# Kernel optimization log

Hardware: AMD Instinct MI355X
Metric: run time of the kernel (lower is better)

The kernel has to match this reference:

```python
import jax, jax.numpy as jnp
import numpy as np

V = 49688; D = 128; Hd = 256; DM = 2 * Hd; FF = 4 * Hd; NH = 4
B = 256; O = 32; L = 32

def _ln(x, g, b, eps=1e-5):
    m = x.mean(-1, keepdims=True)
    v = x.var(-1, keepdims=True)
    return (x - m) / jnp.sqrt(v + eps) * g + b

def _mha(x, in_w, in_b, out_w, out_b, nh):
    Bx, S, E = x.shape
    hd = E // nh
    qkv = x @ in_w.T + in_b
    q, k, v = jnp.split(qkv, 3, axis=-1)
    sp = lambda t: t.reshape(Bx, S, nh, hd).transpose(0, 2, 1, 3)
    q, k, v = sp(q), sp(k), sp(v)
    s = jnp.einsum('bhqd,bhkd->bhqk', q, k) / jnp.sqrt(jnp.asarray(hd, x.dtype))
    o = jnp.einsum('bhqk,bhkd->bhqd', jax.nn.softmax(s, -1), v)
    o = o.transpose(0, 2, 1, 3).reshape(Bx, S, E)
    return o @ out_w.T + out_b

def _gru_dir(x, wih, whh, bih, bhh):
    Bx, T, _ = x.shape
    H = whh.shape[1]
    def step(h, xt):
        gi = xt @ wih.T + bih
        gh = h @ whh.T + bhh
        ir, iz, inn = jnp.split(gi, 3, -1)
        hr, hz, hn = jnp.split(gh, 3, -1)
        r = jax.nn.sigmoid(ir + hr)
        z = jax.nn.sigmoid(iz + hz)
        n = jnp.tanh(inn + r * hn)
        h = (1 - z) * n + z * h
        return h, h
    _, hs = jax.lax.scan(step, jnp.zeros((Bx, H), x.dtype), jnp.swapaxes(x, 0, 1))
    return jnp.swapaxes(hs, 0, 1)

def setup_inputs():
    key = jax.random.key(0)
    it = iter(jax.random.split(key, 48))
    def nrm(shape, s=0.05):
        return jax.random.normal(next(it), shape, jnp.float32) * s
    inp = {}
    inp['order_history'] = jax.random.randint(next(it), (B, O, L), 0, V + 1)
    inp['days_between'] = jax.random.uniform(next(it), (B, O - 1), jnp.float32) * 30.0
    inp['days_since_last'] = jax.random.uniform(next(it), (B,), jnp.float32) * 30.0
    inp['emb'] = nrm((V + 1, D), 1.0).at[0].set(0.0)  # padding_idx=0 -> zero row
    inp['a_in_w'] = nrm((3 * D, D)); inp['a_in_b'] = jnp.zeros((3 * D,))
    inp['a_out_w'] = nrm((D, D)); inp['a_out_b'] = jnp.zeros((D,))
    for d in ('f', 'b'):
        inp['g_wih_' + d] = nrm((3 * Hd, D)); inp['g_whh_' + d] = nrm((3 * Hd, Hd))
        inp['g_bih_' + d] = jnp.zeros((3 * Hd,)); inp['g_bhh_' + d] = jnp.zeros((3 * Hd,))
    inp['t_in_w'] = nrm((3 * DM, DM)); inp['t_in_b'] = jnp.zeros((3 * DM,))
    inp['t_out_w'] = nrm((DM, DM)); inp['t_out_b'] = jnp.zeros((DM,))
    inp['t_ln1_g'] = jnp.ones((DM,)); inp['t_ln1_b'] = jnp.zeros((DM,))
    inp['t_ff1_w'] = nrm((FF, DM)); inp['t_ff1_b'] = jnp.zeros((FF,))
    inp['t_ff2_w'] = nrm((DM, FF)); inp['t_ff2_b'] = jnp.zeros((DM,))
    inp['t_ln2_g'] = jnp.ones((DM,)); inp['t_ln2_b'] = jnp.zeros((DM,))
    inp['te1_w'] = nrm((Hd // 4, 2)); inp['te1_b'] = jnp.zeros((Hd // 4,))
    inp['te_ln1_g'] = jnp.ones((Hd // 4,)); inp['te_ln1_b'] = jnp.zeros((Hd // 4,))
    inp['te2_w'] = nrm((Hd // 2, Hd // 4)); inp['te2_b'] = jnp.zeros((Hd // 2,))
    inp['te_ln2_g'] = jnp.ones((Hd // 2,)); inp['te_ln2_b'] = jnp.zeros((Hd // 2,))
    inp['c_w'] = nrm((Hd, 2 * Hd + Hd // 2)); inp['c_b'] = jnp.zeros((Hd,))
    inp['c_ln_g'] = jnp.ones((Hd,)); inp['c_ln_b'] = jnp.zeros((Hd,))
    return inp

def reference(order_history, days_between, days_since_last, emb, a_in_w, a_in_b, a_out_w, a_out_b, g_wih_f, g_whh_f, g_bih_f, g_bhh_f, g_wih_b, g_whh_b, g_bih_b, g_bhh_b, t_in_w, t_in_b, t_out_w, t_out_b, t_ln1_g, t_ln1_b, t_ff1_w, t_ff1_b, t_ff2_w, t_ff2_b, t_ln2_g, t_ln2_b, te1_w, te1_b, te_ln1_g, te_ln1_b, te2_w, te2_b, te_ln2_g, te_ln2_b, c_w, c_b, c_ln_g, c_ln_b):
    Bx, Ox, Lx = order_history.shape
    # per-order item self-attention, batched over all (user, order) pairs
    x = emb[order_history].reshape(Bx * Ox, Lx, -1)                  # [B*O, L, D]
    x = _mha(x, a_in_w, a_in_b, a_out_w, a_out_b, NH)
    order_emb = x.mean(1).reshape(Bx, Ox, -1)                        # [B, O, D]
    # bidirectional GRU over the order sequence
    hf = _gru_dir(order_emb, g_wih_f, g_whh_f, g_bih_f, g_bhh_f)
    hb = _gru_dir(order_emb[:, ::-1], g_wih_b, g_whh_b, g_bih_b, g_bhh_b)[:, ::-1]
    g = jnp.concatenate([hf, hb], -1)                                # [B, O, 2H]
    # post-LN TransformerEncoderLayer (relu, dropout in eval mode)
    a = _mha(g, t_in_w, t_in_b, t_out_w, t_out_b, NH)
    g = _ln(g + a, t_ln1_g, t_ln1_b)
    f = jax.nn.relu(g @ t_ff1_w.T + t_ff1_b) @ t_ff2_w.T + t_ff2_b
    g = _ln(g + f, t_ln2_g, t_ln2_b)
    enc = g.mean(1)                                                  # [B, 2H]
    # temporal features: only days_mean and recency are used (std computed but unused in original)
    feats = jnp.stack([days_between.mean(1), days_since_last], 1)    # [B, 2]
    te = jax.nn.relu(_ln(feats @ te1_w.T + te1_b, te_ln1_g, te_ln1_b))
    te = jax.nn.relu(_ln(te @ te2_w.T + te2_b, te_ln2_g, te_ln2_b))  # [B, H/2]
    out = jax.nn.relu(_ln(jnp.concatenate([enc, te], 1) @ c_w.T + c_b, c_ln_g, c_ln_b))
    return out                                                       # [B, H]
```

## Files before the change

### kernel.cpp

```cpp
#include <hip/hip_runtime.h>
#include <hip/hip_bf16.h>
#include <math.h>

typedef __hip_bfloat16 bf16;
typedef __attribute__((ext_vector_type(8))) short short8v;
typedef __attribute__((ext_vector_type(4))) short short4v;
typedef __attribute__((ext_vector_type(4))) float float4v;
#define MFMA16 __builtin_amdgcn_mfma_f32_16x16x32_bf16

__device__ __forceinline__ float us2f(unsigned short u) {
  union { unsigned u; float f; } c; c.u = ((unsigned)u) << 16; return c.f;
}
__device__ __forceinline__ unsigned short f2us(float f) {
  return __bfloat16_as_ushort(__float2bfloat16(f));
}

__device__ __forceinline__ float dot_ff(const float* __restrict__ x,
                                        const float* __restrict__ w, int K) {
  const float4* xp = reinterpret_cast<const float4*>(x);
  const float4* wp = reinterpret_cast<const float4*>(w);
  float acc = 0.f;
  const int n = K >> 2;
  for (int i = 0; i < n; ++i) {
    float4 a = xp[i], b = wp[i];
    acc += a.x*b.x + a.y*b.y + a.z*b.z + a.w*b.w;
  }
  return acc;
}

__device__ __forceinline__ float sigm(float x) { return 1.f / (1.f + expf(-x)); }

__global__ void k_canary(float* __restrict__ out) {
  out[blockIdx.x * 256 + threadIdx.x] = 100.0f;
}

__global__ __launch_bounds__(256) void k_cvt(
    const float* __restrict__ a_in_w, const float* __restrict__ t_in_w,
    const float* __restrict__ t_out_w, const float* __restrict__ t_ff1w,
    const float* __restrict__ t_ff2w, const float* __restrict__ a_out_w,
    unsigned short* __restrict__ awb, unsigned short* __restrict__ twb,
    unsigned short* __restrict__ pwb, unsigned short* __restrict__ f1wb,
    unsigned short* __restrict__ f2wb, unsigned short* __restrict__ awb2)
{
  int i = blockIdx.x * 256 + threadIdx.x;
  if (i < 49152)  awb[i] = f2us(a_in_w[i]);
  if (i < 786432) twb[i] = f2us(t_in_w[i]);
  if (i < 262144) pwb[i] = f2us(t_out_w[i]);
  if (i < 524288) f1wb[i] = f2us(t_ff1w[i]);
  if (i < 524288) f2wb[i] = f2us(t_ff2w[i]);
  if (i < 16384)  awb2[i] = f2us(a_out_w[i]);
}

__global__ __launch_bounds__(256) void k_gru_wb(
    const float* __restrict__ wih_f, const float* __restrict__ whh_f,
    const float* __restrict__ wih_b, const float* __restrict__ whh_b,
    unsigned short* __restrict__ whhb, unsigned short* __restrict__ wihb)
{
  int i = blockIdx.x * 256 + threadIdx.x;
  if (i >= 393216) return;
  int dir = i / 196608, r = i % 196608;
  whhb[i] = f2us((dir ? whh_b : whh_f)[r]);
  if (r < 98304) wihb[dir * 98304 + r] = f2us((dir ? wih_b : wih_f)[r]);
}

__global__ __launch_bounds__(256, 4) void k_order_attn(
    const int* __restrict__ oh, const float* __restrict__ emb,
    const unsigned short* __restrict__ awb, const float* __restrict__ in_b,
    const unsigned short* __restrict__ awb2, const float* __restrict__ out_b,
    float* __restrict__ order_emb)
{
  const int bo = blockIdx.x;
  const int tid = threadIdx.x;
  __shared__ int ids[32];
  __shared__ alignas(16) unsigned short xs[32 * 136];
  __shared__ alignas(16) unsigned short qb[32 * 136];
  __shared__ alignas(16) unsigned short kb[32 * 136];
  __shared__ alignas(16) unsigned short vT[128 * 40];
  unsigned short* pb = xs;
  unsigned short* ob = qb;

  const int lane = tid & 63, wave = tid >> 6;
  const int l15 = lane & 15, quad = lane >> 4;

  if (tid < 32) ids[tid] = oh[bo * 32 + tid];
  __syncthreads();
  for (int i = tid; i < 1024; i += 256) {
    int t = i >> 5, d4 = (i & 31) << 2;
    float4 e4 = *reinterpret_cast<const float4*>(emb + (size_t)ids[t] * 128 + d4);
    short4v s; s[0] = f2us(e4.x); s[1] = f2us(e4.y); s[2] = f2us(e4.z); s[3] = f2us(e4.w);
    *reinterpret_cast<short4v*>(xs + t * 136 + d4) = s;
  }
  __syncthreads();
  {
    short8v af[2][4];
#pragma unroll
    for (int mt = 0; mt < 2; ++mt)
#pragma unroll
      for (int kc = 0; kc < 4; ++kc)
        af[mt][kc] = *reinterpret_cast<const short8v*>(
            xs + (mt * 16 + l15) * 136 + kc * 32 + quad * 8);
    for (int ni = 0; ni < 6; ++ni) {
      const int j = (wave + ni * 4) * 16 + l15;
      const unsigned short* wrow = awb + (size_t)j * 128;
      float4v acc0 = {0.f, 0.f, 0.f, 0.f}, acc1 = {0.f, 0.f, 0.f, 0.f};
#pragma unroll
      for (int kc = 0; kc < 4; ++kc) {
        short8v bfr = *reinterpret_cast<const short8v*>(wrow + kc * 32 + quad * 8);
        acc0 = MFMA16(af[0][kc], bfr, acc0, 0, 0, 0);
        acc1 = MFMA16(af[1][kc], bfr, acc1, 0, 0, 0);
      }
      const float bj = in_b[j];
      const int jj = j & 127;
      if (j < 256) {
        unsigned short* dst = (j < 128) ? qb : kb;
#pragma unroll
        for (int r = 0; r < 4; ++r) {
          int t0 = quad * 4 + r;
          dst[t0 * 136 + jj] = f2us(acc0[r] + bj);
          dst[(t0 + 16) * 136 + jj] = f2us(acc1[r] + bj);
        }
      } else {
        short4v s0, s1;
#pragma unroll
        for (int r = 0; r < 4; ++r) { s0[r] = f2us(acc0[r] + bj); s1[r] = f2us(acc1[r] + bj); }
        *reinterpret_cast<short4v*>(vT + jj * 40 + quad * 4) = s0;
        *reinterpret_cast<short4v*>(vT + jj * 40 + 16 + quad * 4) = s1;
      }
    }
  }
  __syncthreads();
  {
    const int h = wave;
    const float scale1 = 0.17677669529663687f;
    short8v qf[2], kf[2];
#pragma unroll
    for (int mt = 0; mt < 2; ++mt)
      qf[mt] = *reinterpret_cast<const short8v*>(qb + (mt * 16 + l15) * 136 + h * 32 + quad * 8);
#pragma unroll
    for (int nt = 0; nt < 2; ++nt)
      kf[nt] = *reinterpret_cast<const short8v*>(kb + (nt * 16 + l15) * 136 + h * 32 + quad * 8);
    float4v sacc[2][2];
#pragma unroll
    for (int mt = 0; mt < 2; ++mt)
#pragma unroll
      for (int nt = 0; nt < 2; ++nt) {
        sacc[mt][nt] = (float4v){0.f, 0.f, 0.f, 0.f};
        sacc[mt][nt] = MFMA16(qf[mt], kf[nt], sacc[mt][nt], 0, 0, 0);
      }
    float inv_reg[2][4];
#pragma unroll
    for (int mt = 0; mt < 2; ++mt)
#pragma unroll
      for (int r = 0; r < 4; ++r) {
        float s0 = sacc[mt][0][r] * scale1;
        float s1 = sacc[mt][1][r] * scale1;
        float mx = fmaxf(s0, s1);
        mx = fmaxf(mx, __shfl_xor(mx, 1));
        mx = fmaxf(mx, __shfl_xor(mx, 2));
        mx = fmaxf(mx, __shfl_xor(mx, 4));
        mx = fmaxf(mx, __shfl_xor(mx, 8));
        float e0 = expf(s0 - mx), e1 = expf(s1 - mx);
        float sm = e0 + e1;
        sm += __shfl_xor(sm, 1);
        sm += __shfl_xor(sm, 2);
        sm += __shfl_xor(sm, 4);
        sm += __shfl_xor(sm, 8);
        inv_reg[mt][r] = 1.f / sm;
        int row = h * 32 + mt * 16 + quad * 4 + r;
        pb[row * 32 + l15] = f2us(e0);
        pb[row * 32 + 16 + l15] = f2us(e1);
      }
    short8v pf[2], vf[2];
#pragma unroll
    for (int mt = 0; mt < 2; ++mt)
      pf[mt] = *reinterpret_cast<const short8v*>(pb + (h * 32 + mt * 16 + l15) * 32 + quad * 8);
#pragma unroll
    for (int nt = 0; nt < 2; ++nt)
      vf[nt] = *reinterpret_cast<const short8v*>(vT + (h * 32 + nt * 16 + l15) * 40 + quad * 8);
    float4v oacc[2][2];
#pragma unroll
    for (int mt = 0; mt < 2; ++mt)
#pragma unroll
      for (int nt = 0; nt < 2; ++nt) {
        oacc[mt][nt] = (float4v){0.f, 0.f, 0.f, 0.f};
        oacc[mt][nt] = MFMA16(pf[mt], vf[nt], oacc[mt][nt], 0, 0, 0);
      }
#pragma unroll
    for (int mt = 0; mt < 2; ++mt)
#pragma unroll
      for (int r = 0; r < 4; ++r) {
        int t = mt * 16 + quad * 4 + r;
        float inv = inv_reg[mt][r];
#pragma unroll
        for (int nt = 0; nt < 2; ++nt)
          ob[t * 136 + h * 32 + nt * 16 + l15] = f2us(oacc[mt][nt][r] * inv);
      }
  }
  __syncthreads();
  {
    float4v acc[2][2];
#pragma unroll
    for (int mt = 0; mt < 2; ++mt)
#pragma unroll
      for (int nt = 0; nt < 2; ++nt) acc[mt][nt] = (float4v){0.f, 0.f, 0.f, 0.f};
#pragma unroll
    for (int kc = 0; kc < 4; ++kc) {
      short8v af0 = *reinterpret_cast<const short8v*>(ob + l15 * 136 + kc * 32 + quad * 8);
      short8v af1 = *reinterpret_cast<const short8v*>(ob + (16 + l15) * 136 + kc * 32 + quad * 8);
#pragma unroll
      for (int nt = 0; nt < 2; ++nt) {
        int j = (wave * 2 + nt) * 16 + l15;
        short8v bfr = *reinterpret_cast<const short8v*>(awb2 + (size_t)j * 128 + kc * 32 + quad * 8);
        acc[0][nt] = MFMA16(af0, bfr, acc[0][nt], 0, 0, 0);
        acc[1][nt] = MFMA16(af1, bfr, acc[1][nt], 0, 0, 0);
      }
    }
#pragma unroll
    for (int nt = 0; nt < 2; ++nt) {
      float part = 0.f;
#pragma unroll
      for (int mt = 0; mt < 2; ++mt)
#pragma unroll
        for (int r = 0; r < 4; ++r) part += acc[mt][nt][r];
      part += __shfl_xor(part, 16);
      part += __shfl_xor(part, 32);
      if (quad == 0) {
        int j = (wave * 2 + nt) * 16 + l15;
        order_emb[(size_t)bo * 128 + j] = part * (1.f / 32.f) + out_b[j];
      }
    }
  }
}

__global__ __launch_bounds__(256, 2) void k_gru_gi(
    const float* __restrict__ oe, const unsigned short* __restrict__ wihb,
    unsigned short* __restrict__ gi)
{
  const int row0 = blockIdx.x * 32, tid = threadIdx.x;
  __shared__ alignas(16) unsigned short xs[32 * 136];
  for (int i = tid; i < 32 * 128; i += 256) {
    int t = i >> 7, d = i & 127;
    xs[t * 136 + d] = f2us(oe[(size_t)(row0 + t) * 128 + d]);
  }
  __syncthreads();
  const int lane = tid & 63, wave = tid >> 6;
  const int l15 = lane & 15, quad = lane >> 4;
  short8v af[2][4];
#pragma unroll
  for (int mt = 0; mt < 2; ++mt)
#pragma unroll
    for (int kc = 0; kc < 4; ++kc)
      af[mt][kc] = *reinterpret_cast<const short8v*>(
          xs + (mt * 16 + l15) * 136 + kc * 32 + quad * 8);
  for (int ni = 0; ni < 24; ++ni) {
    int col = (wave + ni * 4) * 16 + l15;
    const unsigned short* wrow = wihb + (size_t)col * 128;
    float4v a0 = {0.f,0.f,0.f,0.f}, a1 = {0.f,0.f,0.f,0.f};
#pragma unroll
    for (int kc = 0; kc < 4; ++kc) {
      short8v bfr = *reinterpret_cast<const short8v*>(wrow + kc * 32 + quad * 8);
      a0 = MFMA16(af[0][kc], bfr, a0, 0, 0, 0);
      a1 = MFMA16(af[1][kc], bfr, a1, 0, 0, 0);
    }
#pragma unroll
    for (int r = 0; r < 4; ++r) {
      gi[(size_t)(row0 + quad * 4 + r) * 1536 + col] = f2us(a0[r]);
      gi[(size_t)(row0 + quad * 4 + r + 16) * 1536 + col] = f2us(a1[r]);
    }
  }
}

__global__ __launch_bounds__(512, 2) void k_gru_rec(
    const unsigned short* __restrict__ gi, const unsigned short* __restrict__ whhb,
    const float* __restrict__ bih_f, const float* __restrict__ bhh_f,
    const float* __restrict__ bih_b, const float* __restrict__ bhh_b,
    float* __restrict__ g)
{
  const int b0 = blockIdx.x * 2, dir = blockIdx.y;
  const int tid = threadIdx.x;
  const unsigned short* wb = whhb + (size_t)dir * 196608;
  const float* bih = dir ? bih_b : bih_f;
  const float* bhh = dir ? bhh_b : bhh_f;
  __shared__ alignas(16) unsigned short hb[16 * 264];
  __shared__ float pg[2 * 772];
  const int lane = tid & 63, wave = tid >> 6;
  const int l15 = lane & 15, quad = lane >> 4;
  const int j = tid & 255, mb = tid >> 8;
  const float bir = bih[j], biz = bih[256 + j], bin_ = bih[512 + j];
  const float bhr = bhh[j], bhz = bhh[256 + j], bhn  = bhh[512 + j];
  short8v wf[6][8];
  int cols[6];
#pragma unroll
  for (int ni = 0; ni < 6; ++ni) {
    cols[ni] = (wave + ni * 8) * 16 + l15;
#pragma unroll
    for (int kc = 0; kc < 8; ++kc)
      wf[ni][kc] = *reinterpret_cast<const short8v*>(
          wb + (size_t)cols[ni] * 256 + kc * 32 + quad * 8);
  }
  for (int i = tid; i < 16 * 264; i += 512) hb[i] = 0;
  {
    int t0 = dir ? 31 : 0;
    size_t gb0 = ((size_t)(b0 + mb) * 32 + t0) * 1536 + dir * 768;
    (void)gb0;
  }
  int tcur = dir ? 31 : 0;
  size_t gbase = ((size_t)(b0 + mb) * 32 + tcur) * 1536 + dir * 768;
  float gr = us2f(gi[gbase + j]);
  float gz = us2f(gi[gbase + 256 + j]);
  float gn = us2f(gi[gbase + 512 + j]);
  __syncthreads();
  for (int s = 0; s < 32; ++s) {
    float4v acc[6];
#pragma unroll
    for (int ni = 0; ni < 6; ++ni) acc[ni] = (float4v){0.f, 0.f, 0.f, 0.f};
#pragma unroll
    for (int kc = 0; kc < 8; ++kc) {
      short8v af = *reinterpret_cast<const short8v*>(hb + l15 * 264 + kc * 32 + quad * 8);
#pragma unroll
      for (int ni = 0; ni < 6; ++ni)
        acc[ni] = MFMA16(af, wf[ni][kc], acc[ni], 0, 0, 0);
    }
    if (quad == 0) {
#pragma unroll
      for (int ni = 0; ni < 6; ++ni) {
        pg[cols[ni]] = acc[ni][0];
        pg[772 + cols[ni]] = acc[ni][1];
      }
    }
    float gr2 = 0.f, gz2 = 0.f, gn2 = 0.f;
    if (s < 31) {
      int t2 = dir ? (30 - s) : (s + 1);
      size_t gb2 = ((size_t)(b0 + mb) * 32 + t2) * 1536 + dir * 768;
      gr2 = us2f(gi[gb2 + j]);
      gz2 = us2f(gi[gb2 + 256 + j]);
      gn2 = us2f(gi[gb2 + 512 + j]);
    }
    __syncthreads();
    {
      const int tt = dir ? (31 - s) : s;
      float hprev = us2f(hb[mb * 264 + j]);
      float r = sigm(gr + bir + pg[mb * 772 + j] + bhr);
      float z = sigm(gz + biz + pg[mb * 772 + 256 + j] + bhz);
      float n = tanhf(gn + bin_ + r * (pg[mb * 772 + 512 + j] + bhn));
      float nh = (1.f - z) * n + z * hprev;
      hb[mb * 264 + j] = f2us(nh);
      g[((size_t)(b0 + mb) * 32 + tt) * 512 + dir * 256 + j] = nh;
    }
    gr = gr2; gz = gz2; gn = gn2;
    __syncthreads();
  }
}

#define XS2_STR 264

__global__ __launch_bounds__(256, 3) void k_mha2f(
    const float* __restrict__ g, const unsigned short* __restrict__ twb,
    const float* __restrict__ Bv, float* __restrict__ attn)
{
  const int b = blockIdx.x, h = blockIdx.y, tid = threadIdx.x;
  __shared__ alignas(16) unsigned short xs2[32 * XS2_STR];
  __shared__ alignas(16) unsigned short qk[2 * 32 * 136];
  __shared__ alignas(16) unsigned short vT[128 * 40];
  unsigned short* qs = qk;
  unsigned short* ks = qk + 32 * 136;
  float* sc = reinterpret_cast<float*>(xs2);
  unsigned short* pb = xs2 + 2112;
  const int lane = tid & 63, wave = tid >> 6;
  const int l15 = lane & 15, quad = lane >> 4;

  int wrowi[6];
#pragma unroll
  for (int ni = 0; ni < 6; ++ni) {
    int idx = (wave + ni * 4) * 16 + l15;
    int m = idx >> 7, dd = idx & 127;
    wrowi[ni] = m * 512 + h * 128 + dd;
  }
  float4v acc[6][2];
#pragma unroll
  for (int ni = 0; ni < 6; ++ni)
#pragma unroll
    for (int mt = 0; mt < 2; ++mt) acc[ni][mt] = (float4v){0.f, 0.f, 0.f, 0.f};

  for (int half = 0; half < 2; ++half) {
    __syncthreads();
    for (int i = tid; i < 2048; i += 256) {
      int t = i >> 6, c4 = (i & 63) << 2;
      float4 e4 = *reinterpret_cast<const float4*>(
          g + (size_t)b * 16384 + t * 512 + half * 256 + c4);
      short4v s; s[0] = f2us(e4.x); s[1] = f2us(e4.y); s[2] = f2us(e4.z); s[3] = f2us(e4.w);
      *reinterpret_cast<short4v*>(xs2 + t * XS2_STR + c4) = s;
    }
    __syncthreads();
    for (int kl = 0; kl < 2; ++kl) {
      const int kg = half * 2 + kl;
      short8v af[2][4];
#pragma unroll
      for (int mt = 0; mt < 2; ++mt)
#pragma unroll
        for (int u = 0; u < 4; ++u)
          af[mt][u] = *reinterpret_cast<const short8v*>(
              xs2 + (mt * 16 + l15) * XS2_STR + kl * 128 + u * 32 + quad * 8);
#pragma unroll
      for (int ni = 0; ni < 6; ++ni) {
        const unsigned short* wrow = twb + (size_t)wrowi[ni] * 512 + kg * 128;
#pragma unroll
        for (int u = 0; u < 4; ++u) {
          short8v bfr = *reinterpret_cast<const short8v*>(wrow + u * 32 + quad * 8);
          acc[ni][0] = MFMA16(af[0][u], bfr, acc[ni][0], 0, 0, 0);
          acc[ni][1] = MFMA16(af[1][u], bfr, acc[ni][1], 0, 0, 0);
        }
      }
    }
  }
#pragma unroll
  for (int ni = 0; ni < 6; ++ni) {
    int idx = (wave + ni * 4) * 16 + l15;
    int m = idx >> 7, dd = idx & 127;
    float bj = Bv[wrowi[ni]];
    if (m < 2) {
      unsigned short* dst = (m == 0) ? qs : ks;
#pragma unroll
      for (int r = 0; r < 4; ++r) {
        int t0 = quad * 4 + r;
        dst[t0 * 136 + dd] = f2us(acc[ni][0][r] + bj);
        dst[(t0 + 16) * 136 + dd] = f2us(acc[ni][1][r] + bj);
      }
    } else {
      short4v s0, s1;
#pragma unroll
      for (int r = 0; r < 4; ++r) { s0[r] = f2us(acc[ni][0][r] + bj); s1[r] = f2us(acc[ni][1][r] + bj); }
      *reinterpret_cast<short4v*>(vT + dd * 40 + quad * 4) = s0;
      *reinterpret_cast<short4v*>(vT + dd * 40 + 16 + quad * 4) = s1;
    }
  }
  __syncthreads();
  {
    const float scale2 = 0.08838834764831845f;
    const int mt = wave >> 1, nt = wave & 1;
    float4v a = {0.f, 0.f, 0.f, 0.f};
#pragma unroll
    for (int kc = 0; kc < 4; ++kc) {
      short8v qf = *reinterpret_cast<const short8v*>(qs + (mt * 16 + l15) * 136 + kc * 32 + quad * 8);
      short8v kf = *reinterpret_cast<const short8v*>(ks + (nt * 16 + l15) * 136 + kc * 32 + quad * 8);
      a = MFMA16(qf, kf, a, 0, 0, 0);
    }
#pragma unroll
    for (int r = 0; r < 4; ++r)
      sc[(mt * 16 + quad * 4 + r) * 33 + nt * 16 + l15] = a[r] * scale2;
  }
  __syncthreads();
  if (tid < 128) {
    int row = tid >> 2, seg = tid & 3;
    float* srow = sc + row * 33;
    float mx = srow[seg * 8];
#pragma unroll
    for (int c = 1; c < 8; ++c) mx = fmaxf(mx, srow[seg * 8 + c]);
    mx = fmaxf(mx, __shfl_xor(mx, 1));
    mx = fmaxf(mx, __shfl_xor(mx, 2));
    float s = 0.f;
    short8v pv;
#pragma unroll
    for (int c = 0; c < 8; ++c) {
      float e = expf(srow[seg * 8 + c] - mx);
      s += e; pv[c] = f2us(e);
    }
    *reinterpret_cast<short8v*>(pb + row * 32 + seg * 8) = pv;
    s += __shfl_xor(s, 1);
    s += __shfl_xor(s, 2);
    if (seg == 0) srow[32] = 1.f / s;
  }
  __syncthreads();
  {
    short8v pf[2], vf[2];
#pragma unroll
    for (int mt = 0; mt < 2; ++mt)
      pf[mt] = *reinterpret_cast<const short8v*>(pb + (mt * 16 + l15) * 32 + quad * 8);
#pragma unroll
    for (int ntl = 0; ntl < 2; ++ntl)
      vf[ntl] = *reinterpret_cast<const short8v*>(vT + ((2 * wave + ntl) * 16 + l15) * 40 + quad * 8);
    float4v oacc[2][2];
#pragma unroll
    for (int mt = 0; mt < 2; ++mt)
#pragma unroll
      for (int ntl = 0; ntl < 2; ++ntl) {
        oacc[mt][ntl] = (float4v){0.f, 0.f, 0.f, 0.f};
        oacc[mt][ntl] = MFMA16(pf[mt], vf[ntl], oacc[mt][ntl], 0, 0, 0);
      }
#pragma unroll
    for (int mt = 0; mt < 2; ++mt)
#pragma unroll
      for (int r = 0; r < 4; ++r) {
        int q = mt * 16 + quad * 4 + r;
        float inv = sc[q * 33 + 32];
#pragma unroll
        for (int ntl = 0; ntl < 2; ++ntl)
          attn[((size_t)b * 32 + q) * 512 + h * 128 + (2 * wave + ntl) * 16 + l15] =
              oacc[mt][ntl][r] * inv;
      }
  }
}

__global__ __launch_bounds__(256, 2) void k_projln_mfma(
    const float* __restrict__ X, const unsigned short* __restrict__ Wb,
    const float* __restrict__ bias, const float* __restrict__ res,
    const float* __restrict__ gam, const float* __restrict__ bet,
    float* __restrict__ Y)
{
  const int row0 = blockIdx.x * 16, tid = threadIdx.x;
  __shared__ alignas(16) unsigned short xs[16 * 520];
  __shared__ float ys[16 * 516];
  for (int i = tid; i < 16 * 512; i += 256) {
    int t = i >> 9, c = i & 511;
    xs[t * 520 + c] = f2us(X[(size_t)(row0 + t) * 512 + c]);
  }
  __syncthreads();
  {
    const int lane = tid & 63, wave = tid >> 6;
    const int l15 = lane & 15, quad = lane >> 4;
    short8v af[16];
#pragma unroll
    for (int kc = 0; kc < 16; ++kc)
      af[kc] = *reinterpret_cast<const short8v*>(xs + l15 * 520 + kc * 32 + quad * 8);
    for (int ni = 0; ni < 8; ++ni) {
      int col = (wave + ni * 4) * 16 + l15;
      const unsigned short* wrow = Wb + (size_t)col * 512;
      float4v acc = {0.f,0.f,0.f,0.f};
#pragma unroll
      for (int kc = 0; kc < 16; ++kc) {
        short8v bfr = *reinterpret_cast<const short8v*>(wrow + kc * 32 + quad * 8);
        acc = MFMA16(af[kc], bfr, acc, 0, 0, 0);
      }
      float bj = bias[col];
#pragma unroll
      for (int r = 0; r < 4; ++r)
        ys[(quad * 4 + r) * 516 + col] = acc[r] + bj;
    }
  }
  __syncthreads();
  for (int i = tid; i < 16 * 512; i += 256) {
    int t = i >> 9, c = i & 511;
    ys[t * 516 + c] += res[(size_t)(row0 + t) * 512 + c];
  }
  __syncthreads();
  {
    int row = tid >> 4, l16 = tid & 15;
    const float* yr = ys + row * 516;
    float part = 0.f;
#pragma unroll
    for (int k = 0; k < 32; ++k) part += yr[l16 + 16 * k];
#pragma unroll
    for (int off = 8; off; off >>= 1) part += __shfl_xor(part, off, 16);
    float mean = part * (1.f / 512.f);
    float var = 0.f;
#pragma unroll
    for (int k = 0; k < 32; ++k) { float d = yr[l16 + 16 * k] - mean; var += d * d; }
#pragma unroll
    for (int off = 8; off; off >>= 1) var += __shfl_xor(var, off, 16);
    float rs = rsqrtf(var * (1.f / 512.f) + 1e-5f);
    for (int k = 0; k < 32; ++k) {
      int c = l16 + 16 * k;
      Y[(size_t)(row0 + row) * 512 + c] = (yr[c] - mean) * rs * gam[c] + bet[c];
    }
  }
}

__global__ __launch_bounds__(256, 2) void k_ff1_mfma(
    const float* __restrict__ X, const unsigned short* __restrict__ Wb,
    const float* __restrict__ bias, unsigned short* __restrict__ Y)
{
  const int row0 = blockIdx.x * 16, tid = threadIdx.x;
  __shared__ alignas(16) unsigned short xs[16 * 520];
  for (int i = tid; i < 16 * 512; i += 256) {
    int t = i >> 9, c = i & 511;
    xs[t * 520 + c] = f2us(X[(size_t)(row0 + t) * 512 + c]);
  }
  __syncthreads();
  const int lane = tid & 63, wave = tid >> 6;
  const int l15 = lane & 15, quad = lane >> 4;
  short8v af[16];
#pragma unroll
  for (int kc = 0; kc < 16; ++kc)
    af[kc] = *reinterpret_cast<const short8v*>(xs + l15 * 520 + kc * 32 + quad * 8);
  for (int ni = 0; ni < 16; ++ni) {
    int col = (wave + ni * 4) * 16 + l15;
    const unsigned short* wrow = Wb + (size_t)col * 512;
    float4v acc = {0.f,0.f,0.f,0.f};
#pragma unroll
    for (int kc = 0; kc < 16; ++kc) {
      short8v bfr = *reinterpret_cast<const short8v*>(wrow + kc * 32 + quad * 8);
      acc = MFMA16(af[kc], bfr, acc, 0, 0, 0);
    }
    float bj = bias[col];
#pragma unroll
    for (int r = 0; r < 4; ++r)
      Y[(size_t)(row0 + quad * 4 + r) * 1024 + col] = f2us(fmaxf(acc[r] + bj, 0.f));
  }
}

__global__ __launch_bounds__(256, 2) void k_ff2ln_mfma(
    const unsigned short* __restrict__ X, const unsigned short* __restrict__ Wb,
    const float* __restrict__ bias, const float* __restrict__ res,
    const float* __restrict__ gam, const float* __restrict__ bet,
    float* __restrict__ Y)
{
  const int row0 = blockIdx.x * 16, tid = threadIdx.x;
  __shared__ alignas(16) unsigned short xs[16 * 520];
  __shared__ float ys[16 * 516];
  const int lane = tid & 63, wave = tid >> 6;
  const int l15 = lane & 15, quad = lane >> 4;
  float4v acc[8];
#pragma unroll
  for (int ni = 0; ni < 8; ++ni) acc[ni] = (float4v){0.f,0.f,0.f,0.f};
  for (int half = 0; half < 2; ++half) {
    __syncthreads();
    for (int i = tid; i < 16 * 512; i += 256) {
      int t = i >> 9, c = i & 511;
      xs[t * 520 + c] = X[(size_t)(row0 + t) * 1024 + half * 512 + c];
    }
    __syncthreads();
    short8v af[16];
#pragma unroll
    for (int kc = 0; kc < 16; ++kc)
      af[kc] = *reinterpret_cast<const short8v*>(xs + l15 * 520 + kc * 32 + quad * 8);
#pragma unroll
    for (int ni = 0; ni < 8; ++ni) {
      int col = (wave + ni * 4) * 16 + l15;
      const unsigned short* wrow = Wb + (size_t)col * 1024 + half * 512;
#pragma unroll
      for (int kc = 0; kc < 16; ++kc) {
        short8v bfr = *reinterpret_cast<const short8v*>(wrow + kc * 32 + quad * 8);
        acc[ni] = MFMA16(af[kc], bfr, acc[ni], 0, 0, 0);
      }
    }
  }
  __syncthreads();
  for (int ni = 0; ni < 8; ++ni) {
    int col = (wave + ni * 4) * 16 + l15;
    float bj = bias[col];
#pragma unroll
    for (int r = 0; r < 4; ++r)
      ys[(quad * 4 + r) * 516 + col] = acc[ni][r] + bj;
  }
  __syncthreads();
  for (int i = tid; i < 16 * 512; i += 256) {
    int t = i >> 9, c = i & 511;
    ys[t * 516 + c] += res[(size_t)(row0 + t) * 512 + c];
  }
  __syncthreads();
  {
    int row = tid >> 4, l16 = tid & 15;
    const float* yr = ys + row * 516;
    float part = 0.f;
#pragma unroll
    for (int k = 0; k < 32; ++k) part += yr[l16 + 16 * k];
#pragma unroll
    for (int off = 8; off; off >>= 1) part += __shfl_xor(part, off, 16);
    float mean = part * (1.f / 512.f);
    float var = 0.f;
#pragma unroll
    for (int k = 0; k < 32; ++k) { float d = yr[l16 + 16 * k] - mean; var += d * d; }
#pragma unroll
    for (int off = 8; off; off >>= 1) var += __shfl_xor(var, off, 16);
    float rs = rsqrtf(var * (1.f / 512.f) + 1e-5f);
    for (int k = 0; k < 32; ++k) {
      int c = l16 + 16 * k;
      Y[(size_t)(row0 + row) * 512 + c] = (yr[c] - mean) * rs * gam[c] + bet[c];
    }
  }
}

__global__ __launch_bounds__(256) void k_final(
    const float* __restrict__ g2,
    const float* __restrict__ db, const float* __restrict__ dsl,
    const float* __restrict__ te1_w, const float* __restrict__ te1_b,
    const float* __restrict__ l1g, const float* __restrict__ l1b,
    const float* __restrict__ te2_w, const float* __restrict__ te2_b,
    const float* __restrict__ l2g, const float* __restrict__ l2b,
    const float* __restrict__ c_w, const float* __restrict__ c_b,
    const float* __restrict__ clg, const float* __restrict__ clb,
    float* __restrict__ out)
{
  const int b = blockIdx.x, tid = threadIdx.x;
  __shared__ float cat[640];
  __shared__ float t1[64];
  __shared__ float t2[128];
  __shared__ float pre[256];
  __shared__ float red[256];
  __shared__ float st[2];
  for (int i = tid; i < 512; i += 256) {
    float acc = 0.f;
#pragma unroll
    for (int t = 0; t < 32; ++t) acc += g2[((size_t)b * 32 + t) * 512 + i];
    cat[i] = acc * (1.f / 32.f);
  }
  if (tid == 0) {
    float s = 0.f;
    for (int i = 0; i < 31; ++i) s += db[b * 31 + i];
    st[0] = s / 31.f;
    st[1] = dsl[b];
  }
  __syncthreads();
  const float f0 = st[0], f1v = st[1];
  if (tid < 64)
    t1[tid] = f0 * te1_w[tid * 2] + f1v * te1_w[tid * 2 + 1] + te1_b[tid];
  __syncthreads();
  if (tid == 0) {
    float m = 0.f; for (int i = 0; i < 64; ++i) m += t1[i]; m *= (1.f / 64.f);
    float v = 0.f; for (int i = 0; i < 64; ++i) { float d = t1[i] - m; v += d * d; }
    st[0] = m; st[1] = rsqrtf(v * (1.f / 64.f) + 1e-5f);
  }
  __syncthreads();
  if (tid < 64) {
    float v = (t1[tid] - st[0]) * st[1] * l1g[tid] + l1b[tid];
    t1[tid] = fmaxf(v, 0.f);
  }
  __syncthreads();
  if (tid < 128)
    t2[tid] = dot_ff(t1, te2_w + (size_t)tid * 64, 64) + te2_b[tid];
  __syncthreads();
  if (tid == 0) {
    float m = 0.f; for (int i = 0; i < 128; ++i) m += t2[i]; m *= (1.f / 128.f);
    float v = 0.f; for (int i = 0; i < 128; ++i) { float d = t2[i] - m; v += d * d; }
    st[0] = m; st[1] = rsqrtf(v * (1.f / 128.f) + 1e-5f);
  }
  __syncthreads();
  if (tid < 128) {
    float v = (t2[tid] - st[0]) * st[1] * l2g[tid] + l2b[tid];
    cat[512 + tid] = fmaxf(v, 0.f);
  }
  __syncthreads();
  pre[tid] = dot_ff(cat, c_w + (size_t)tid * 640, 640) + c_b[tid];
  red[tid] = pre[tid];
  __syncthreads();
  for (int s = 128; s > 0; s >>= 1) { if (tid < s) red[tid] += red[tid + s]; __syncthreads(); }
  const float m = red[0] * (1.f / 256.f);
  __syncthreads();
  const float d = pre[tid] - m;
  red[tid] = d * d;
  __syncthreads();
  for (int s = 128; s > 0; s >>= 1) { if (tid < s) red[tid] += red[tid + s]; __syncthreads(); }
  const float rs = rsqrtf(red[0] * (1.f / 256.f) + 1e-5f);
  float v = d * rs * clg[tid] + clb[tid];
  out[(size_t)b * 256 + tid] = fmaxf(v, 0.f);
}

extern "C" void kernel_launch(void* const* d_in, const int* in_sizes, int n_in,
                              void* d_out, int out_size, void* d_ws, size_t ws_size,
                              hipStream_t stream) {
  (void)in_sizes; (void)n_in; (void)out_size; (void)ws_size;
  const int*   oh     = (const int*)  d_in[0];
  const float* db     = (const float*)d_in[1];
  const float* dsl    = (const float*)d_in[2];
  const float* emb    = (const float*)d_in[3];
  const float* a_in_w = (const float*)d_in[4];
  const float* a_in_b = (const float*)d_in[5];
  const float* a_out_w= (const float*)d_in[6];
  const float* a_out_b= (const float*)d_in[7];
  const float* wih_f  = (const float*)d_in[8];
  const float* whh_f  = (const float*)d_in[9];
  const float* bih_f  = (const float*)d_in[10];
  const float* bhh_f  = (const float*)d_in[11];
  const float* wih_b  = (const float*)d_in[12];
  const float* whh_b  = (const float*)d_in[13];
  const float* bih_b  = (const float*)d_in[14];
  const float* bhh_b  = (const float*)d_in[15];
  const float* t_in_w = (const float*)d_in[16];
  const float* t_in_b = (const float*)d_in[17];
  const float* t_out_w= (const float*)d_in[18];
  const float* t_out_b= (const float*)d_in[19];
  const float* t_ln1g = (const float*)d_in[20];
  const float* t_ln1b = (const float*)d_in[21];
  const float* t_ff1w = (const float*)d_in[22];
  const float* t_ff1b = (const float*)d_in[23];
  const float* t_ff2w = (const float*)d_in[24];
  const float* t_ff2b = (const float*)d_in[25];
  const float* t_ln2g = (const float*)d_in[26];
  const float* t_ln2b = (const float*)d_in[27];
  const float* te1_w  = (const float*)d_in[28];
  const float* te1_b  = (const float*)d_in[29];
  const float* tl1g   = (const float*)d_in[30];
  const float* tl1b   = (const float*)d_in[31];
  const float* te2_w  = (const float*)d_in[32];
  const float* te2_b  = (const float*)d_in[33];
  const float* tl2g   = (const float*)d_in[34];
  const float* tl2b   = (const float*)d_in[35];
  const float* c_w    = (const float*)d_in[36];
  const float* c_b    = (const float*)d_in[37];
  const float* clng   = (const float*)d_in[38];
  const float* clnb   = (const float*)d_in[39];

  float* ws = (float*)d_ws;
  float* oe   = ws;
  float* g    = ws + 1048576;
  float* attn = ws + 5242880;
  float* g1   = attn;
  unsigned short* f1 = (unsigned short*)(ws + 1048576);
  float* g2   = ws + 1048576;
  unsigned short* whhb = (unsigned short*)(ws + 9437184);
  unsigned short* wihb = (unsigned short*)(ws + 9633792);
  unsigned short* awb2 = (unsigned short*)(ws + 9732096);
  unsigned short* awb  = (unsigned short*)(ws + 10027008);
  unsigned short* twb  = (unsigned short*)(ws + 10051584);
  unsigned short* pwb  = (unsigned short*)(ws + 10444800);
  unsigned short* f1wb = (unsigned short*)(ws + 10575872);
  unsigned short* f2wb = (unsigned short*)(ws + 10838016);
  unsigned short* gi   = (unsigned short*)(ws + 11100160);

  k_canary<<<256, 256, 0, stream>>>((float*)d_out);
  k_cvt<<<3072, 256, 0, stream>>>(a_in_w, t_in_w, t_out_w, t_ff1w, t_ff2w, a_out_w,
                                  awb, twb, pwb, f1wb, f2wb, awb2);
  k_gru_wb<<<1536, 256, 0, stream>>>(wih_f, whh_f, wih_b, whh_b, whhb, wihb);
  k_order_attn<<<8192, 256, 0, stream>>>(oh, emb, awb, a_in_b, awb2, a_out_b, oe);
  k_gru_gi<<<256, 256, 0, stream>>>(oe, wihb, gi);
  k_gru_rec<<<dim3(128, 2), 512, 0, stream>>>(gi, whhb, bih_f, bhh_f, bih_b, bhh_b, g);
  k_mha2f<<<dim3(256, 4), 256, 0, stream>>>(g, twb, t_in_b, attn);
  k_projln_mfma<<<512, 256, 0, stream>>>(attn, pwb, t_out_b, g, t_ln1g, t_ln1b, g1);
  k_ff1_mfma<<<512, 256, 0, stream>>>(g1, f1wb, t_ff1b, f1);
  k_ff2ln_mfma<<<512, 256, 0, stream>>>(f1, f2wb, t_ff2b, g1, t_ln2g, t_ln2b, g2);
  k_final<<<256, 256, 0, stream>>>(g2, db, dsl, te1_w, te1_b, tl1g, tl1b,
                                   te2_w, te2_b, tl2g, tl2b, c_w, c_b, clng, clnb,
                                   (float*)d_out);
}
```

Baseline: 635.5 us.

## Pre-convert embedding table to bf16, store order embedding as bf16, fuse FF layers

```diff
diff --git a/kernel.cpp b/kernel.cpp
--- a/kernel.cpp
+++ b/kernel.cpp
@@ -38,11 +38,18 @@
     const float* __restrict__ a_in_w, const float* __restrict__ t_in_w,
     const float* __restrict__ t_out_w, const float* __restrict__ t_ff1w,
     const float* __restrict__ t_ff2w, const float* __restrict__ a_out_w,
+    const float* __restrict__ emb,
     unsigned short* __restrict__ awb, unsigned short* __restrict__ twb,
     unsigned short* __restrict__ pwb, unsigned short* __restrict__ f1wb,
-    unsigned short* __restrict__ f2wb, unsigned short* __restrict__ awb2)
+    unsigned short* __restrict__ f2wb, unsigned short* __restrict__ awb2,
+    unsigned short* __restrict__ embb)
 {
   int i = blockIdx.x * 256 + threadIdx.x;
+  if (i < 1590048) {
+    float4 e4 = *reinterpret_cast<const float4*>(emb + (size_t)i * 4);
+    short4v s; s[0] = f2us(e4.x); s[1] = f2us(e4.y); s[2] = f2us(e4.z); s[3] = f2us(e4.w);
+    *reinterpret_cast<short4v*>(embb + (size_t)i * 4) = s;
+  }
   if (i < 49152)  awb[i] = f2us(a_in_w[i]);
   if (i < 786432) twb[i] = f2us(t_in_w[i]);
   if (i < 262144) pwb[i] = f2us(t_out_w[i]);
@@ -64,10 +71,10 @@
 }
 
 __global__ __launch_bounds__(256, 4) void k_order_attn(
-    const int* __restrict__ oh, const float* __restrict__ emb,
+    const int* __restrict__ oh, const unsigned short* __restrict__ embb,
     const unsigned short* __restrict__ awb, const float* __restrict__ in_b,
     const unsigned short* __restrict__ awb2, const float* __restrict__ out_b,
-    float* __restrict__ order_emb)
+    unsigned short* __restrict__ oeb)
 {
   const int bo = blockIdx.x;
   const int tid = threadIdx.x;
@@ -84,11 +91,10 @@
 
   if (tid < 32) ids[tid] = oh[bo * 32 + tid];
   __syncthreads();
-  for (int i = tid; i < 1024; i += 256) {
-    int t = i >> 5, d4 = (i & 31) << 2;
-    float4 e4 = *reinterpret_cast<const float4*>(emb + (size_t)ids[t] * 128 + d4);
-    short4v s; s[0] = f2us(e4.x); s[1] = f2us(e4.y); s[2] = f2us(e4.z); s[3] = f2us(e4.w);
-    *reinterpret_cast<short4v*>(xs + t * 136 + d4) = s;
+  for (int i = tid; i < 512; i += 256) {
+    int t = i >> 4, c8 = (i & 15) << 3;
+    *reinterpret_cast<short8v*>(xs + t * 136 + c8) =
+        *reinterpret_cast<const short8v*>(embb + (size_t)ids[t] * 128 + c8);
   }
   __syncthreads();
   {
@@ -226,21 +232,22 @@
       part += __shfl_xor(part, 32);
       if (quad == 0) {
         int j = (wave * 2 + nt) * 16 + l15;
-        order_emb[(size_t)bo * 128 + j] = part * (1.f / 32.f) + out_b[j];
+        oeb[(size_t)bo * 128 + j] = f2us(part * (1.f / 32.f) + out_b[j]);
       }
     }
   }
 }
 
 __global__ __launch_bounds__(256, 2) void k_gru_gi(
-    const float* __restrict__ oe, const unsigned short* __restrict__ wihb,
+    const unsigned short* __restrict__ oeb, const unsigned short* __restrict__ wihb,
     unsigned short* __restrict__ gi)
 {
   const int row0 = blockIdx.x * 32, tid = threadIdx.x;
   __shared__ alignas(16) unsigned short xs[32 * 136];
-  for (int i = tid; i < 32 * 128; i += 256) {
-    int t = i >> 7, d = i & 127;
-    xs[t * 136 + d] = f2us(oe[(size_t)(row0 + t) * 128 + d]);
+  for (int i = tid; i < 512; i += 256) {
+    int t = i >> 4, c8 = (i & 15) << 3;
+    *reinterpret_cast<short8v*>(xs + t * 136 + c8) =
+        *reinterpret_cast<const short8v*>(oeb + (size_t)(row0 + t) * 128 + c8);
   }
   __syncthreads();
   const int lane = tid & 63, wave = tid >> 6;
@@ -299,11 +306,6 @@
           wb + (size_t)cols[ni] * 256 + kc * 32 + quad * 8);
   }
   for (int i = tid; i < 16 * 264; i += 512) hb[i] = 0;
-  {
-    int t0 = dir ? 31 : 0;
-    size_t gb0 = ((size_t)(b0 + mb) * 32 + t0) * 1536 + dir * 768;
-    (void)gb0;
-  }
   int tcur = dir ? 31 : 0;
   size_t gbase = ((size_t)(b0 + mb) * 32 + tcur) * 1536 + dir * 768;
   float gr = us2f(gi[gbase + j]);
@@ -565,82 +567,72 @@
   }
 }
 
-__global__ __launch_bounds__(256, 2) void k_ff1_mfma(
-    const float* __restrict__ X, const unsigned short* __restrict__ Wb,
-    const float* __restrict__ bias, unsigned short* __restrict__ Y)
-{
-  const int row0 = blockIdx.x * 16, tid = threadIdx.x;
-  __shared__ alignas(16) unsigned short xs[16 * 520];
-  for (int i = tid; i < 16 * 512; i += 256) {
-    int t = i >> 9, c = i & 511;
-    xs[t * 520 + c] = f2us(X[(size_t)(row0 + t) * 512 + c]);
-  }
-  __syncthreads();
-  const int lane = tid & 63, wave = tid >> 6;
-  const int l15 = lane & 15, quad = lane >> 4;
-  short8v af[16];
-#pragma unroll
-  for (int kc = 0; kc < 16; ++kc)
-    af[kc] = *reinterpret_cast<const short8v*>(xs + l15 * 520 + kc * 32 + quad * 8);
-  for (int ni = 0; ni < 16; ++ni) {
-    int col = (wave + ni * 4) * 16 + l15;
-    const unsigned short* wrow = Wb + (size_t)col * 512;
-    float4v acc = {0.f,0.f,0.f,0.f};
-#pragma unroll
-    for (int kc = 0; kc < 16; ++kc) {
-      short8v bfr = *reinterpret_cast<const short8v*>(wrow + kc * 32 + quad * 8);
-      acc = MFMA16(af[kc], bfr, acc, 0, 0, 0);
-    }
-    float bj = bias[col];
-#pragma unroll
-    for (int r = 0; r < 4; ++r)
-      Y[(size_t)(row0 + quad * 4 + r) * 1024 + col] = f2us(fmaxf(acc[r] + bj, 0.f));
-  }
-}
-
-__global__ __launch_bounds__(256, 2) void k_ff2ln_mfma(
-    const unsigned short* __restrict__ X, const unsigned short* __restrict__ Wb,
-    const float* __restrict__ bias, const float* __restrict__ res,
+__global__ __launch_bounds__(256, 3) void k_ffln(
+    const float* __restrict__ X, const unsigned short* __restrict__ W1,
+    const float* __restrict__ b1, const unsigned short* __restrict__ W2,
+    const float* __restrict__ b2, const float* __restrict__ res,
     const float* __restrict__ gam, const float* __restrict__ bet,
     float* __restrict__ Y)
 {
   const int row0 = blockIdx.x * 16, tid = threadIdx.x;
   __shared__ alignas(16) unsigned short xs[16 * 520];
-  __shared__ float ys[16 * 516];
+  __shared__ alignas(16) unsigned short f1L[16 * 1032];
+  float* ys = reinterpret_cast<float*>(f1L);
   const int lane = tid & 63, wave = tid >> 6;
   const int l15 = lane & 15, quad = lane >> 4;
-  float4v acc[8];
-#pragma unroll
-  for (int ni = 0; ni < 8; ++ni) acc[ni] = (float4v){0.f,0.f,0.f,0.f};
-  for (int half = 0; half < 2; ++half) {
-    __syncthreads();
-    for (int i = tid; i < 16 * 512; i += 256) {
-      int t = i >> 9, c = i & 511;
-      xs[t * 520 + c] = X[(size_t)(row0 + t) * 1024 + half * 512 + c];
-    }
-    __syncthreads();
+  for (int i = tid; i < 16 * 512; i += 256) {
+    int t = i >> 9, c = i & 511;
+    xs[t * 520 + c] = f2us(X[(size_t)(row0 + t) * 512 + c]);
+  }
+  __syncthreads();
+  {
     short8v af[16];
 #pragma unroll
     for (int kc = 0; kc < 16; ++kc)
       af[kc] = *reinterpret_cast<const short8v*>(xs + l15 * 520 + kc * 32 + quad * 8);
+    for (int ni = 0; ni < 16; ++ni) {
+      int col = (wave + ni * 4) * 16 + l15;
+      const unsigned short* wrow = W1 + (size_t)col * 512;
+      float4v acc = {0.f,0.f,0.f,0.f};
+#pragma unroll
+      for (int kc = 0; kc < 16; ++kc) {
+        short8v bfr = *reinterpret_cast<const short8v*>(wrow + kc * 32 + quad * 8);
+        acc = MFMA16(af[kc], bfr, acc, 0, 0, 0);
+      }
+      float bj = b1[col];
+#pragma unroll
+      for (int r = 0; r < 4; ++r)
+        f1L[(quad * 4 + r) * 1032 + col] = f2us(fmaxf(acc[r] + bj, 0.f));
+    }
+  }
+  __syncthreads();
+  float4v acc2[8];
+#pragma unroll
+  for (int ni = 0; ni < 8; ++ni) acc2[ni] = (float4v){0.f,0.f,0.f,0.f};
+  for (int half = 0; half < 2; ++half) {
+    short8v af[16];
+#pragma unroll
+    for (int kc = 0; kc < 16; ++kc)
+      af[kc] = *reinterpret_cast<const short8v*>(
+          f1L + l15 * 1032 + half * 512 + kc * 32 + quad * 8);
 #pragma unroll
     for (int ni = 0; ni < 8; ++ni) {
       int col = (wave + ni * 4) * 16 + l15;
-      const unsigned short* wrow = Wb + (size_t)col * 1024 + half * 512;
+      const unsigned short* wrow = W2 + (size_t)col * 1024 + half * 512;
 #pragma unroll
       for (int kc = 0; kc < 16; ++kc) {
         short8v bfr = *reinterpret_cast<const short8v*>(wrow + kc * 32 + quad * 8);
-        acc[ni] = MFMA16(af[kc], bfr, acc[ni], 0, 0, 0);
+        acc2[ni] = MFMA16(af[kc], bfr, acc2[ni], 0, 0, 0);
       }
     }
   }
   __syncthreads();
   for (int ni = 0; ni < 8; ++ni) {
     int col = (wave + ni * 4) * 16 + l15;
-    float bj = bias[col];
+    float bj = b2[col];
 #pragma unroll
     for (int r = 0; r < 4; ++r)
-      ys[(quad * 4 + r) * 516 + col] = acc[ni][r] + bj;
+      ys[(quad * 4 + r) * 516 + col] = acc2[ni][r] + bj;
   }
   __syncthreads();
   for (int i = tid; i < 16 * 512; i += 256) {
@@ -791,11 +783,11 @@
   const float* clnb   = (const float*)d_in[39];
 
   float* ws = (float*)d_ws;
-  float* oe   = ws;
+  unsigned short* oeb = (unsigned short*)ws;
+  unsigned short* embb= (unsigned short*)(ws + 1048576);
   float* g    = ws + 1048576;
   float* attn = ws + 5242880;
   float* g1   = attn;
-  unsigned short* f1 = (unsigned short*)(ws + 1048576);
   float* g2   = ws + 1048576;
   unsigned short* whhb = (unsigned short*)(ws + 9437184);
   unsigned short* wihb = (unsigned short*)(ws + 9633792);
@@ -808,16 +800,16 @@
   unsigned short* gi   = (unsigned short*)(ws + 11100160);
 
   k_canary<<<256, 256, 0, stream>>>((float*)d_out);
-  k_cvt<<<3072, 256, 0, stream>>>(a_in_w, t_in_w, t_out_w, t_ff1w, t_ff2w, a_out_w,
-                                  awb, twb, pwb, f1wb, f2wb, awb2);
+  k_cvt<<<6212, 256, 0, stream>>>(a_in_w, t_in_w, t_out_w, t_ff1w, t_ff2w, a_out_w,
+                                  emb, awb, twb, pwb, f1wb, f2wb, awb2, embb);
   k_gru_wb<<<1536, 256, 0, stream>>>(wih_f, whh_f, wih_b, whh_b, whhb, wihb);
-  k_order_attn<<<8192, 256, 0, stream>>>(oh, emb, awb, a_in_b, awb2, a_out_b, oe);
-  k_gru_gi<<<256, 256, 0, stream>>>(oe, wihb, gi);
+  k_order_attn<<<8192, 256, 0, stream>>>(oh, embb, awb, a_in_b, awb2, a_out_b, oeb);
+  k_gru_gi<<<256, 256, 0, stream>>>(oeb, wihb, gi);
   k_gru_rec<<<dim3(128, 2), 512, 0, stream>>>(gi, whhb, bih_f, bhh_f, bih_b, bhh_b, g);
   k_mha2f<<<dim3(256, 4), 256, 0, stream>>>(g, twb, t_in_b, attn);
   k_projln_mfma<<<512, 256, 0, stream>>>(attn, pwb, t_out_b, g, t_ln1g, t_ln1b, g1);
-  k_ff1_mfma<<<512, 256, 0, stream>>>(g1, f1wb, t_ff1b, f1);
-  k_ff2ln_mfma<<<512, 256, 0, stream>>>(f1, f2wb, t_ff2b, g1, t_ln2g, t_ln2b, g2);
+  k_ffln<<<512, 256, 0, stream>>>(g1, f1wb, t_ff1b, f2wb, t_ff2b, g1,
+                                  t_ln2g, t_ln2b, g2);
   k_final<<<256, 256, 0, stream>>>(g2, db, dsl, te1_w, te1_b, tl1g, tl1b,
                                    te2_w, te2_b, tl2g, tl2b, c_w, c_b, clng, clnb,
                                    (float*)d_out);
```

New measurement: 658.2 us. +3.6%, slower.
